# Performance work log

Hardware: AMD Instinct MI355X
Metric: run time of the kernel (lower is better)

## Reference

```python
import jax, jax.numpy as jnp
import numpy as np

B, S, D, H, W = 2, 2048, 1024, 16, 128
HD = D // H


def setup_inputs() -> dict:
    key = jax.random.key(0)
    ks = jax.random.split(key, 9)
    s = 1.0 / np.sqrt(D)
    return {
        "x": jax.random.normal(ks[0], (B, S, D), jnp.float32),
        "Wq": jax.random.normal(ks[1], (D, D), jnp.float32) * s,
        "bq": jax.random.normal(ks[2], (D,), jnp.float32) * 0.01,
        "Wk": jax.random.normal(ks[3], (D, D), jnp.float32) * s,
        "bk": jax.random.normal(ks[4], (D,), jnp.float32) * 0.01,
        "Wv": jax.random.normal(ks[5], (D, D), jnp.float32) * s,
        "bv": jax.random.normal(ks[6], (D,), jnp.float32) * 0.01,
        "Wo": jax.random.normal(ks[7], (D, D), jnp.float32) * s,
        "bo": jax.random.normal(ks[8], (D,), jnp.float32) * 0.01,
    }


def reference(x, Wq, bq, Wk, bk, Wv, bv, Wo, bo):
    b, s, d = x.shape
    # projections (torch Linear: x @ W.T + b)
    q = (jnp.einsum('bsd,ed->bse', x, Wq) + bq).reshape(b, s, H, HD).transpose(0, 2, 1, 3)
    k = (jnp.einsum('bsd,ed->bse', x, Wk) + bk).reshape(b, s, H, HD).transpose(0, 2, 1, 3)
    v = (jnp.einsum('bsd,ed->bse', x, Wv) + bv).reshape(b, s, H, HD).transpose(0, 2, 1, 3)
    scores = jnp.einsum('bhqd,bhkd->bhqk', q, k) / jnp.sqrt(jnp.asarray(HD, x.dtype))
    # local band mask: mask[i, j] = 1 iff i - W//2 <= j <= i + W//2
    idx = jnp.arange(s)
    band = jnp.abs(idx[:, None] - idx[None, :]) <= (W // 2)  # [S, S]
    scores = jnp.where(band[None, None], scores, -jnp.inf)
    attn = jax.nn.softmax(scores, axis=-1)  # dropout is identity in eval
    ctx = jnp.einsum('bhqk,bhkd->bqhd', attn, v).reshape(b, s, d)
    out = jnp.einsum('bsd,ed->bse', ctx, Wo) + bo
    return out, attn
```

## Files before the change

### kernel.cpp

```cpp
#include <hip/hip_runtime.h>
#include <math.h>
#include <stdint.h>

typedef _Float16 f16;
typedef f16   f16x8 __attribute__((ext_vector_type(8)));
typedef f16   f16x4 __attribute__((ext_vector_type(4)));
typedef float f32x4 __attribute__((ext_vector_type(4)));

constexpr int Bc = 2, Sc = 2048, Dc = 1024, Hc = 16, HDc = 64;
constexpr size_t PROJ = (size_t)Bc * Sc * Dc;
constexpr size_t WN   = (size_t)Dc * Dc;

__device__ __forceinline__ void gload_lds16(const void* g, void* l) {
    unsigned int off = (unsigned int)(uintptr_t)l;
    auto lp = (__attribute__((address_space(3))) unsigned int*)(uintptr_t)off;
    auto gp = (const __attribute__((address_space(1))) unsigned int*)(uintptr_t)g;
    __builtin_amdgcn_global_load_lds(gp, lp, 16, 0, 0);
}

__device__ __forceinline__ void fill_rows32(float* __restrict__ attn, int grow0, int t) {
    const uint4 z = {0u, 0u, 0u, 0u};
    for (int rr = 0; rr < 32; ++rr) {
        const int gr = grow0 + rr;
        const int i = gr & (Sc - 1);
        const int lo = (i > 64) ? (i - 64) : 0;
        const int a0 = lo & ~31;
        const int hi = (i < Sc - 65) ? (i + 64) : (Sc - 1);
        int a1 = (hi + 32) & ~31; if (a1 > Sc) a1 = Sc;
        uint4* rowp = (uint4*)(attn + (size_t)gr * Sc);
        const int n4L = a0 >> 2;
        const int r0  = a1 >> 2;
        const int tot = n4L + (512 - r0);
        for (int idx = t; idx < tot; idx += 256) {
            const int p = (idx < n4L) ? idx : (r0 + idx - n4L);
            rowp[p] = z;
        }
    }
}

__global__ __launch_bounds__(256)
void pack_all(const float* __restrict__ x,
              const float* __restrict__ w0, const float* __restrict__ w1,
              const float* __restrict__ w2, const float* __restrict__ w3,
              f16* __restrict__ xd, f16* __restrict__ wd) {
    const int bid = blockIdx.x;
    const float* src;
    f16* dst;
    int off4;
    if (bid < 4096) {
        src = x; dst = xd; off4 = bid;
    } else {
        const int wi = (bid - 4096) >> 10;
        const int r  = (bid - 4096) & 1023;
        src = (wi == 0) ? w0 : (wi == 1) ? w1 : (wi == 2) ? w2 : w3;
        dst = wd + (size_t)wi * WN;
        off4 = r;
    }
    const int i = off4 * 256 + threadIdx.x;
    float4 f = ((const float4*)src)[i];
    f16x4 h = {(f16)f.x, (f16)f.y, (f16)f.z, (f16)f.w};
    ((f16x4*)dst)[i] = h;
}

template <typename OutT, bool WITH_FILL>
__global__ __launch_bounds__(256, 2)
void gemm_mega(const f16* __restrict__ A, const f16* __restrict__ W,
               const float* __restrict__ b0, const float* __restrict__ b1,
               const float* __restrict__ b2,
               OutT* __restrict__ o0, OutT* __restrict__ o1, OutT* __restrict__ o2,
               float* __restrict__ fill, int n_ct) {
    constexpr int K = 1024, N = 1024;
    const int bid = blockIdx.x;
    const int t = threadIdx.x;

    int gid = bid;
    if (WITH_FILL) {
        int fid = -1;
        if (bid < 1536) {
            const int g8 = bid >> 3, l8 = bid & 7;
            if (g8 & 1) fid = (g8 >> 1) * 8 + l8;
            else        gid = (g8 >> 1) * 8 + l8;
        } else {
            fid = 768 + (bid - 1536);
        }
        if (fid >= 0) {
            fill_rows32(fill, fid * 32, t);
            return;
        }
    }

    __shared__ f16 sA[128 * 32];
    __shared__ f16 sB[128 * 32];

    const int w = t >> 6, l = t & 63, l15 = l & 15, quad = l >> 4;
    const int col_t = gid % n_ct, row_t = gid / n_ct;
    const int row0 = row_t * 128, col0 = col_t * 128;
    const int wr = w >> 1, wc = w & 1;

    f32x4 acc[4][4];
    #pragma unroll
    for (int i = 0; i < 4; ++i)
        #pragma unroll
        for (int j = 0; j < 4; ++j) acc[i][j] = (f32x4){0.f, 0.f, 0.f, 0.f};

    const int arow = t >> 2;
    const int koff = (t & 3) * 8;
    const f16* ga = A + (size_t)(row0 + arow) * K + koff;
    const f16* gb = W + (size_t)(col0 + arow) * K + koff;
    f16* lA1 = sA + w * 512;
    f16* lA2 = sA + 2048 + w * 512;
    f16* lB1 = sB + w * 512;
    f16* lB2 = sB + 2048 + w * 512;

    for (int k0 = 0; k0 < K; k0 += 32) {
        gload_lds16(ga + k0, lA1);
        gload_lds16(ga + (size_t)64 * K + k0, lA2);
        gload_lds16(gb + k0, lB1);
        gload_lds16(gb + (size_t)64 * K + k0, lB2);
        __syncthreads();

        f16x8 af[4], bf[4];
        #pragma unroll
        for (int mi = 0; mi < 4; ++mi)
            af[mi] = *(const f16x8*)&sA[(wr * 64 + mi * 16 + l15) * 32 + quad * 8];
        #pragma unroll
        for (int ni = 0; ni < 4; ++ni)
            bf[ni] = *(const f16x8*)&sB[(wc * 64 + ni * 16 + l15) * 32 + quad * 8];
        #pragma unroll
        for (int mi = 0; mi < 4; ++mi)
            #pragma unroll
            for (int ni = 0; ni < 4; ++ni)
                acc[mi][ni] = __builtin_amdgcn_mfma_f32_16x16x32_f16(af[mi], bf[ni], acc[mi][ni], 0, 0, 0);
        __syncthreads();
    }

    const int ten = col0 >> 10;
    const float* bias = (ten == 0) ? b0 : (ten == 1) ? b1 : b2;
    OutT* out = (ten == 0) ? o0 : (ten == 1) ? o1 : o2;
    const int nc0 = col0 & (N - 1);

    #pragma unroll
    for (int mi = 0; mi < 4; ++mi)
        #pragma unroll
        for (int ni = 0; ni < 4; ++ni) {
            const int rbase = row0 + wr * 64 + mi * 16 + quad * 4;
            const int col = nc0 + wc * 64 + ni * 16 + l15;
            const float bv = bias[col];
            #pragma unroll
            for (int r = 0; r < 4; ++r)
                out[(size_t)(rbase + r) * N + col] = (OutT)(acc[mi][ni][r] + bv);
        }
}

__global__ __launch_bounds__(256, 2)
void attn_fused(const f16* __restrict__ qb, const f16* __restrict__ kb,
                const f16* __restrict__ vb, float* __restrict__ attn,
                f16* __restrict__ ctx) {
    const int bid = blockIdx.x;
    const int t = threadIdx.x;

    int aid = bid, fid = -1;
    if (bid < 1536) {
        const int g8 = bid >> 3, l8 = bid & 7;
        if (g8 & 1) fid = (g8 >> 1) * 8 + l8;
        else        aid = (g8 >> 1) * 8 + l8;
    } else {
        aid = 768 + (bid - 1536);
    }
    if (fid >= 0) {
        fill_rows32(attn, 40960 + fid * 32, t);
        return;
    }

    __shared__ f16 sQ[64 * 72];
    __shared__ f16 sK[192 * 72];
    __shared__ f16 sV[192 * 72];
    f16* sP = sK;

    const int w = t >> 6, l = t & 63, l15 = l & 15, quad = l >> 4;
    const int tile = aid & 31, h = (aid >> 5) & 15, b = aid >> 9;
    const int q0 = tile * 64;
    const int jbase = q0 - 64;

    const f16* qg = qb + ((size_t)(b * Sc + q0)) * Dc + h * HDc;
    #pragma unroll
    for (int it = 0; it < 2; ++it) {
        const int idx = it * 256 + t;
        const int r = idx >> 3, c = (idx & 7) * 8;
        *(uint4*)&sQ[r * 72 + c] = *(const uint4*)&qg[(size_t)r * Dc + c];
    }
    #pragma unroll
    for (int it = 0; it < 6; ++it) {
        const int idx = it * 256 + t;
        const int r = idx >> 3, c = (idx & 7) * 8;
        int j = jbase + r;
        j = (j < 0) ? 0 : (j > Sc - 1 ? Sc - 1 : j);
        const size_t goff = ((size_t)(b * Sc + j)) * Dc + h * HDc + c;
        *(uint4*)&sK[r * 72 + c] = *(const uint4*)&kb[goff];
        *(uint4*)&sV[r * 72 + c] = *(const uint4*)&vb[goff];
    }
    __syncthreads();

    f32x4 s[12];
    #pragma unroll
    for (int nt = 0; nt < 12; ++nt) s[nt] = (f32x4){0.f, 0.f, 0.f, 0.f};
    #pragma unroll
    for (int kk = 0; kk < 64; kk += 32) {
        const f16x8 aq = *(const f16x8*)&sQ[(w * 16 + l15) * 72 + kk + quad * 8];
        #pragma unroll
        for (int nt = 0; nt < 12; ++nt) {
            const f16x8 bk_ = *(const f16x8*)&sK[(nt * 16 + l15) * 72 + kk + quad * 8];
            s[nt] = __builtin_amdgcn_mfma_f32_16x16x32_f16(aq, bk_, s[nt], 0, 0, 0);
        }
    }

    float invr[4];
    #pragma unroll
    for (int r = 0; r < 4; ++r) {
        const int row = w * 16 + quad * 4 + r;
        const int lo = (row > 64 - q0) ? row : (64 - q0);
        const int hi2 = (row + 128 < 2111 - q0) ? (row + 128) : (2111 - q0);
        float m = -1e30f;
        #pragma unroll
        for (int nt = 0; nt < 12; ++nt) {
            const int jrel = nt * 16 + l15;
            const float v = s[nt][r] * 0.125f;
            if (jrel >= lo && jrel <= hi2) m = fmaxf(m, v);
        }
        #pragma unroll
        for (int k = 1; k < 16; k <<= 1) m = fmaxf(m, __shfl_xor(m, k, 64));
        float sum = 0.f;
        #pragma unroll
        for (int nt = 0; nt < 12; ++nt) {
            const int jrel = nt * 16 + l15;
            const float v = s[nt][r] * 0.125f;
            const float e = (jrel >= lo && jrel <= hi2) ? __expf(v - m) : 0.f;
            s[nt][r] = e;
            sum += e;
        }
        #pragma unroll
        for (int k = 1; k < 16; k <<= 1) sum += __shfl_xor(sum, k, 64);
        invr[r] = 1.f / sum;
    }
    __syncthreads();

    float* abase = attn + ((size_t)(b * Hc + h) * Sc) * Sc;
    #pragma unroll
    for (int r = 0; r < 4; ++r) {
        const int row = w * 16 + quad * 4 + r;
        const int i = q0 + row;
        const int lo0 = (i > 64) ? (i - 64) : 0;
        const int a0 = lo0 & ~31;
        const int hi0 = (i < Sc - 65) ? (i + 64) : (Sc - 1);
        int a1 = (hi0 + 32) & ~31; if (a1 > Sc) a1 = Sc;
        const int alo = a0 - jbase, ahi = a1 - jbase;
        #pragma unroll
        for (int nt = 0; nt < 12; ++nt) {
            const int jrel = nt * 16 + l15;
            const float p = s[nt][r] * invr[r];
            sP[row * 200 + jrel] = (f16)p;
            if (jrel >= alo && jrel < ahi)
                abase[(size_t)i * Sc + (jbase + jrel)] = p;
        }
    }
    __syncthreads();

    f32x4 o[4];
    #pragma unroll
    for (int dt = 0; dt < 4; ++dt) o[dt] = (f32x4){0.f, 0.f, 0.f, 0.f};
    #pragma unroll
    for (int ks = 0; ks < 6; ++ks) {
        const f16x8 ap = *(const f16x8*)&sP[(w * 16 + l15) * 200 + ks * 32 + quad * 8];
        #pragma unroll
        for (int dt = 0; dt < 4; ++dt) {
            f16x8 bv;
            #pragma unroll
            for (int jj = 0; jj < 8; ++jj)
                bv[jj] = sV[(ks * 32 + quad * 8 + jj) * 72 + dt * 16 + l15];
            o[dt] = __builtin_amdgcn_mfma_f32_16x16x32_f16(ap, bv, o[dt], 0, 0, 0);
        }
    }
    f16* cg = ctx + ((size_t)(b * Sc + q0)) * Dc + h * HDc;
    #pragma unroll
    for (int dt = 0; dt < 4; ++dt)
        #pragma unroll
        for (int r = 0; r < 4; ++r) {
            const int row = w * 16 + quad * 4 + r;
            cg[(size_t)row * Dc + dt * 16 + l15] = (f16)o[dt][r];
        }
}

extern "C" void kernel_launch(void* const* d_in, const int* in_sizes, int n_in,
                              void* d_out, int out_size, void* d_ws, size_t ws_size,
                              hipStream_t stream) {
    const float* x  = (const float*)d_in[0];
    const float* Wq = (const float*)d_in[1];
    const float* bq = (const float*)d_in[2];
    const float* Wk = (const float*)d_in[3];
    const float* bk = (const float*)d_in[4];
    const float* Wv = (const float*)d_in[5];
    const float* bv = (const float*)d_in[6];
    const float* Wo = (const float*)d_in[7];
    const float* bo = (const float*)d_in[8];

    float* out  = (float*)d_out;
    float* attn = out + PROJ;

    char* ws = (char*)d_ws;
    f16* Wcat  = (f16*)ws;
    f16* x_f16 = (f16*)(ws + (size_t)8  * 1024 * 1024);
    f16* q_f16 = (f16*)(ws + (size_t)16 * 1024 * 1024);
    f16* k_f16 = (f16*)(ws + (size_t)24 * 1024 * 1024);
    f16* v_f16 = (f16*)(ws + (size_t)32 * 1024 * 1024);
    f16* c_f16 = (f16*)(ws + (size_t)40 * 1024 * 1024);

    pack_all<<<dim3(8192), dim3(256), 0, stream>>>(x, Wq, Wk, Wv, Wo, x_f16, Wcat);

    gemm_mega<f16, true><<<dim3(2048), dim3(256), 0, stream>>>(
        x_f16, Wcat, bq, bk, bv, q_f16, k_f16, v_f16, attn, 24);

    attn_fused<<<dim3(1792), dim3(256), 0, stream>>>(
        q_f16, k_f16, v_f16, attn, c_f16);

    gemm_mega<float, false><<<dim3(256), dim3(256), 0, stream>>>(
        c_f16, Wcat + 3 * WN, bo, bo, bo, out, out, out, nullptr, 8);
}
```

Measured before the change: 647.6 us.

## Write V transposed from projection GEMM to enable vectorized PV operand loads

The QKV projection epilogue now writes V in a per-(batch, dim) transposed layout with token as the fastest axis, and zero-pads guard regions before and after it. The attention kernel loads V^T rows into shared memory and reads the PV MFMA B-operand as one 16-byte vector instead of eight strided scalar LDS reads. The cost moves into the GEMM epilogue, which now does strided 8-byte global stores, and out-of-range halo tokens read the zeroed padding instead of clamped rows.

After: 644.7 us. Within noise of the previous version (-0.5%).

```diff
diff --git a/kernel.cpp b/kernel.cpp
--- a/kernel.cpp
+++ b/kernel.cpp
@@ -42,8 +42,17 @@
 void pack_all(const float* __restrict__ x,
               const float* __restrict__ w0, const float* __restrict__ w1,
               const float* __restrict__ w2, const float* __restrict__ w3,
-              f16* __restrict__ xd, f16* __restrict__ wd) {
+              f16* __restrict__ xd, f16* __restrict__ wd, f16* __restrict__ vT) {
     const int bid = blockIdx.x;
+    if (bid == 8192) {
+        const uint4 z = {0u, 0u, 0u, 0u};
+        uint4* pre  = (uint4*)(vT - 256);
+        uint4* post = (uint4*)(vT + (size_t)4 * 1024 * 1024);
+        const int t = threadIdx.x;
+        if (t < 32) pre[t] = z;
+        else if (t < 64) post[t - 32] = z;
+        return;
+    }
     const float* src;
     f16* dst;
     int off4;
@@ -139,6 +148,25 @@
     OutT* out = (ten == 0) ? o0 : (ten == 1) ? o1 : o2;
     const int nc0 = col0 & (N - 1);
 
+    if constexpr (WITH_FILL) {
+        if (ten == 2) {
+            f16* vout = reinterpret_cast<f16*>(o2);
+            #pragma unroll
+            for (int mi = 0; mi < 4; ++mi)
+                #pragma unroll
+                for (int ni = 0; ni < 4; ++ni) {
+                    const int tok  = row0 + wr * 64 + mi * 16 + quad * 4;
+                    const int colv = nc0 + wc * 64 + ni * 16 + l15;
+                    const float bvv = bias[colv];
+                    f16x4 h4 = {(f16)(acc[mi][ni][0] + bvv), (f16)(acc[mi][ni][1] + bvv),
+                                (f16)(acc[mi][ni][2] + bvv), (f16)(acc[mi][ni][3] + bvv)};
+                    const int bb = tok >> 11;
+                    *(f16x4*)&vout[((size_t)(bb * 1024 + colv)) * 2048 + (tok & 2047)] = h4;
+                }
+            return;
+        }
+    }
+
     #pragma unroll
     for (int mi = 0; mi < 4; ++mi)
         #pragma unroll
@@ -154,7 +182,7 @@
 
 __global__ __launch_bounds__(256, 2)
 void attn_fused(const f16* __restrict__ qb, const f16* __restrict__ kb,
-                const f16* __restrict__ vb, float* __restrict__ attn,
+                const f16* __restrict__ vT, float* __restrict__ attn,
                 f16* __restrict__ ctx) {
     const int bid = blockIdx.x;
     const int t = threadIdx.x;
@@ -174,7 +202,7 @@
 
     __shared__ f16 sQ[64 * 72];
     __shared__ f16 sK[192 * 72];
-    __shared__ f16 sV[192 * 72];
+    __shared__ f16 sVT[64 * 200];
     f16* sP = sK;
 
     const int w = t >> 6, l = t & 63, l15 = l & 15, quad = l >> 4;
@@ -197,7 +225,15 @@
         j = (j < 0) ? 0 : (j > Sc - 1 ? Sc - 1 : j);
         const size_t goff = ((size_t)(b * Sc + j)) * Dc + h * HDc + c;
         *(uint4*)&sK[r * 72 + c] = *(const uint4*)&kb[goff];
-        *(uint4*)&sV[r * 72 + c] = *(const uint4*)&vb[goff];
+    }
+    {
+        const f16* vrow = vT + ((size_t)((b * Hc + h) * HDc)) * Sc + jbase;
+        const int dd = t >> 2;
+        #pragma unroll
+        for (int it = 0; it < 6; ++it) {
+            const int ch = it * 4 + (t & 3);
+            *(uint4*)&sVT[dd * 200 + ch * 8] = *(const uint4*)&vrow[(size_t)dd * Sc + ch * 8];
+        }
     }
     __syncthreads();
 
@@ -273,10 +309,7 @@
         const f16x8 ap = *(const f16x8*)&sP[(w * 16 + l15) * 200 + ks * 32 + quad * 8];
         #pragma unroll
         for (int dt = 0; dt < 4; ++dt) {
-            f16x8 bv;
-            #pragma unroll
-            for (int jj = 0; jj < 8; ++jj)
-                bv[jj] = sV[(ks * 32 + quad * 8 + jj) * 72 + dt * 16 + l15];
+            const f16x8 bv = *(const f16x8*)&sVT[(dt * 16 + l15) * 200 + ks * 32 + quad * 8];
             o[dt] = __builtin_amdgcn_mfma_f32_16x16x32_f16(ap, bv, o[dt], 0, 0, 0);
         }
     }
@@ -311,16 +344,16 @@
     f16* x_f16 = (f16*)(ws + (size_t)8  * 1024 * 1024);
     f16* q_f16 = (f16*)(ws + (size_t)16 * 1024 * 1024);
     f16* k_f16 = (f16*)(ws + (size_t)24 * 1024 * 1024);
-    f16* v_f16 = (f16*)(ws + (size_t)32 * 1024 * 1024);
     f16* c_f16 = (f16*)(ws + (size_t)40 * 1024 * 1024);
-
-    pack_all<<<dim3(8192), dim3(256), 0, stream>>>(x, Wq, Wk, Wv, Wo, x_f16, Wcat);
+    f16* vT    = (f16*)(ws + (size_t)48 * 1024 * 1024 + 512);
+
+    pack_all<<<dim3(8193), dim3(256), 0, stream>>>(x, Wq, Wk, Wv, Wo, x_f16, Wcat, vT);
 
     gemm_mega<f16, true><<<dim3(2048), dim3(256), 0, stream>>>(
-        x_f16, Wcat, bq, bk, bv, q_f16, k_f16, v_f16, attn, 24);
+        x_f16, Wcat, bq, bk, bv, q_f16, k_f16, vT, attn, 24);
 
     attn_fused<<<dim3(1792), dim3(256), 0, stream>>>(
-        q_f16, k_f16, v_f16, attn, c_f16);
+        q_f16, k_f16, vT, attn, c_f16);
 
     gemm_mega<float, false><<<dim3(256), dim3(256), 0, stream>>>(
         c_f16, Wcat + 3 * WN, bo, bo, bo, out, out, out, nullptr, 8);
```
